# Kernel tuning notes

Hardware: AMD Instinct MI355X
Metric: run time of the kernel (lower is better)

## Reference

```python
import jax, jax.numpy as jnp
import numpy as np
from jax import lax

DILATIONS = (1, 3, 5)
EPS = 1e-5
B, T, C, S, K = 8, 4096, 512, 64, 3


def _adain(x, s, w, b):
    # instance norm over time (axis=1), per (batch, channel), no learned affine;
    # style-conditioned affine: (1+gamma)*xn + beta
    h = s @ w + b                              # (B, 2C)
    gamma, beta = jnp.split(h, 2, axis=-1)     # (B, C) each
    mu = jnp.mean(x, axis=1, keepdims=True)
    var = jnp.var(x, axis=1, keepdims=True)
    xn = (x - mu) * lax.rsqrt(var + EPS)
    return (1.0 + gamma[:, None, :]) * xn + beta[:, None, :]


def _snake(x, alpha):
    # snake activation: x + (1/a) * sin(a*x)^2
    return x + (1.0 / alpha) * jnp.sin(alpha * x) ** 2


def _wn_conv(x, v, g, b, dilation):
    # weight-normalized dilated 1d conv; v: (K, Cin, Cout), norm over (K, Cin)
    norm = jnp.sqrt(jnp.sum(v * v, axis=(0, 1), keepdims=True))
    w = g[None, None, :] * v / norm
    y = lax.conv_general_dilated(x, w, window_strides=(1,), padding='SAME',
                                 rhs_dilation=(dilation,),
                                 dimension_numbers=('NWC', 'WIO', 'NWC'))
    return y + b


def setup_inputs() -> dict:
    key = jax.random.key(0)
    ks = jax.random.split(key, 6)
    return {
        'x': jax.random.normal(ks[0], (B, T, C), dtype=jnp.float32),
        's': jax.random.normal(ks[1], (B, S), dtype=jnp.float32),
        'fc1_w': jax.random.normal(ks[2], (3, S, 2 * C), dtype=jnp.float32) * 0.02,
        'fc1_b': jnp.zeros((3, 2 * C), dtype=jnp.float32),
        'alpha1': jnp.ones((3, 1, 1, C), dtype=jnp.float32),
        'conv1_v': jax.random.normal(ks[3], (3, K, C, C), dtype=jnp.float32),
        'conv1_g': jnp.ones((3, C), dtype=jnp.float32),
        'conv1_b': jnp.zeros((3, C), dtype=jnp.float32),
        'fc2_w': jax.random.normal(ks[4], (3, S, 2 * C), dtype=jnp.float32) * 0.02,
        'fc2_b': jnp.zeros((3, 2 * C), dtype=jnp.float32),
        'alpha2': jnp.ones((3, 1, 1, C), dtype=jnp.float32),
        'conv2_v': jax.random.normal(ks[5], (3, K, C, C), dtype=jnp.float32),
        'conv2_g': jnp.ones((3, C), dtype=jnp.float32),
        'conv2_b': jnp.zeros((3, C), dtype=jnp.float32),
    }


def reference(x, s, fc1_w, fc1_b, alpha1, conv1_v, conv1_g, conv1_b,
              fc2_w, fc2_b, alpha2, conv2_v, conv2_g, conv2_b):
    for i, d in enumerate(DILATIONS):
        xt = _adain(x, s, fc1_w[i], fc1_b[i])
        xt = _snake(xt, alpha1[i])
        xt = _wn_conv(xt, conv1_v[i], conv1_g[i], conv1_b[i], d)
        xt = _adain(xt, s, fc2_w[i], fc2_b[i])
        xt = _snake(xt, alpha2[i])
        xt = _wn_conv(xt, conv2_v[i], conv2_g[i], conv2_b[i], 1)
        x = xt + x
    return x
```

## Files before the change

### kernel.cpp

```cpp
#include <hip/hip_runtime.h>
#include <hip/hip_bf16.h>

#define B_ 8
#define T_ 4096
#define C_ 512
#define S_ 64
#define KT 3
#define EPSC 1e-5f

typedef __attribute__((ext_vector_type(8))) short bf16x8;
typedef __attribute__((ext_vector_type(4))) float f32x4;

__device__ inline unsigned short f2bf(float x) {
    __hip_bfloat16 h = __float2bfloat16(x);
    return *reinterpret_cast<unsigned short*>(&h);
}

__global__ void norm_partial(const float* __restrict__ v1, const float* __restrict__ v2,
                             float* __restrict__ normsq) {
    int j = blockIdx.y;
    int i = j >> 1;
    const float* v = ((j & 1) ? v2 : v1) + (size_t)i * KT * C_ * C_;
    int r0 = blockIdx.x * 16;
    int tid = threadIdx.x;
    float a0 = 0.f, a1 = 0.f;
    for (int r = 0; r < 16; ++r) {
        const float* row = v + (size_t)(r0 + r) * C_;
        float x = row[tid];
        float y = row[tid + 256];
        a0 += x * x; a1 += y * y;
    }
    atomicAdd(&normsq[j * C_ + tid], a0);
    atomicAdd(&normsq[j * C_ + tid + 256], a1);
}

__global__ void wt_kernel(const float* __restrict__ v1, const float* __restrict__ v2,
                          const float* __restrict__ g1, const float* __restrict__ g2,
                          const float* __restrict__ normsq, unsigned short* __restrict__ wT) {
    __shared__ float tile[64][65];
    int jk = blockIdx.y;
    int j = jk / 3, k = jk % 3;
    int i = j >> 1;
    const float* v = ((j & 1) ? v2 : v1) + ((size_t)i * KT + k) * C_ * C_;
    const float* g = ((j & 1) ? g2 : g1) + (size_t)i * C_;
    int tci = (blockIdx.x >> 3) * 64;
    int tco = (blockIdx.x & 7) * 64;
    int tid = threadIdx.x;
    int lr = tid >> 6, lc = tid & 63;
    for (int rr = 0; rr < 16; ++rr) {
        int ci = rr * 4 + lr;
        tile[ci][lc] = v[(size_t)(tci + ci) * C_ + tco + lc];
    }
    __syncthreads();
    for (int rr = 0; rr < 16; ++rr) {
        int co_l = rr * 4 + lr;
        int co = tco + co_l;
        float w = g[co] * rsqrtf(normsq[j * C_ + co]) * tile[lc][co_l];
        wT[((size_t)j * KT + k) * C_ * C_ + (size_t)co * C_ + tci + lc] = f2bf(w);
    }
}

__global__ void stats_partial(const float* __restrict__ u, float* __restrict__ ssum,
                              float* __restrict__ ssq) {
    int c = blockIdx.y * 256 + threadIdx.x;
    int b = blockIdx.z;
    int t0 = blockIdx.x * 64;
    const float* p = u + ((size_t)b * T_ + t0) * C_ + c;
    float s1 = 0.f, s2 = 0.f;
    for (int t = 0; t < 64; ++t) {
        float x = p[(size_t)t * C_];
        s1 += x; s2 += x * x;
    }
    atomicAdd(&ssum[b * C_ + c], s1);
    atomicAdd(&ssq[b * C_ + c], s2);
}

__global__ void adain_finalize(const float* __restrict__ ssum, const float* __restrict__ ssq,
                               const float* __restrict__ s, const float* __restrict__ fcw,
                               const float* __restrict__ fcb,
                               float* __restrict__ scale, float* __restrict__ shift) {
    int idx = blockIdx.x * 256 + threadIdx.x;
    int b = idx >> 9, c = idx & (C_ - 1);
    float mu = ssum[idx] * (1.f / T_);
    float var = ssq[idx] * (1.f / T_) - mu * mu;
    var = fmaxf(var, 0.f);
    float gamma = fcb[c], beta = fcb[C_ + c];
    const float* sp = s + b * S_;
    for (int p = 0; p < S_; ++p) {
        float sv = sp[p];
        gamma += sv * fcw[p * 2 * C_ + c];
        beta  += sv * fcw[p * 2 * C_ + C_ + c];
    }
    float sc = (1.f + gamma) * rsqrtf(var + EPSC);
    scale[idx] = sc;
    shift[idx] = beta - mu * sc;
}

__global__ void act_kernel(const float* __restrict__ u, const float* __restrict__ scale,
                           const float* __restrict__ shift, const float* __restrict__ alpha,
                           unsigned short* __restrict__ z) {
    size_t idx4 = (size_t)blockIdx.x * 256 + threadIdx.x;
    size_t e0 = idx4 * 4;
    int c = (int)(e0 & (C_ - 1));
    int b = (int)(e0 >> 21);
    const float4 xv = *(const float4*)(u + e0);
    const float4 scv = *(const float4*)(scale + b * C_ + c);
    const float4 shv = *(const float4*)(shift + b * C_ + c);
    const float4 av = *(const float4*)(alpha + c);
    float xx[4] = {xv.x, xv.y, xv.z, xv.w};
    float ss[4] = {scv.x, scv.y, scv.z, scv.w};
    float hh[4] = {shv.x, shv.y, shv.z, shv.w};
    float aa[4] = {av.x, av.y, av.z, av.w};
    ushort4 o;
    unsigned short r[4];
    #pragma unroll
    for (int q = 0; q < 4; ++q) {
        float val = xx[q] * ss[q] + hh[q];
        float sn = sinf(aa[q] * val);
        r[q] = f2bf(val + sn * sn / aa[q]);
    }
    o.x = r[0]; o.y = r[1]; o.z = r[2]; o.w = r[3];
    *(ushort4*)(z + e0) = o;
}

#define BM 128
#define BN 128
#define HALO 5
#define AROWS (BM + 2 * HALO)
#define LSTR 40

__global__ __launch_bounds__(256) void conv_kernel(
    const unsigned short* __restrict__ z, const unsigned short* __restrict__ wT,
    const float* __restrict__ bias, const float* __restrict__ residual,
    float* __restrict__ out, int dil) {
    __shared__ unsigned short As[AROWS * LSTR];
    __shared__ unsigned short Bs[3 * BN * LSTR];
    int tid = threadIdx.x;
    int m0 = blockIdx.x * BM;
    int b = m0 >> 12;
    int t0 = m0 & (T_ - 1);
    int n0 = blockIdx.y * BN;
    int wv = tid >> 6;
    int l = tid & 63;
    int wm = (wv >> 1) * 64, wn = (wv & 1) * 64;
    int l16 = l & 15, lg = l >> 4;
    int ar = tid >> 2;
    int acol = (tid & 3) * 8;

    f32x4 acc[4][4];
    #pragma unroll
    for (int a = 0; a < 4; ++a)
        #pragma unroll
        for (int q = 0; q < 4; ++q) acc[a][q] = (f32x4){0.f, 0.f, 0.f, 0.f};

    for (int cc = 0; cc < C_; cc += 32) {
        #pragma unroll
        for (int it = 0; it < 3; ++it) {
            int r = ar + it * 64;
            if (r < AROWS) {
                int t = t0 - HALO + r;
                uint4 val = make_uint4(0u, 0u, 0u, 0u);
                if (t >= 0 && t < T_)
                    val = *(const uint4*)(z + ((size_t)b * T_ + t) * C_ + cc + acol);
                *(uint4*)(&As[r * LSTR + acol]) = val;
            }
        }
        #pragma unroll
        for (int it = 0; it < 6; ++it) {
            int r = ar + it * 64;
            int k = r >> 7, co = (r & 127) + n0;
            uint4 val = *(const uint4*)(wT + ((size_t)k * C_ + co) * C_ + cc + acol);
            *(uint4*)(&Bs[r * LSTR + acol]) = val;
        }
        __syncthreads();

        #pragma unroll
        for (int k = 0; k < 3; ++k) {
            int sh = (k - 1) * dil + HALO;
            bf16x8 afr[4], bfr[4];
            #pragma unroll
            for (int mf = 0; mf < 4; ++mf) {
                int row = wm + mf * 16 + l16 + sh;
                afr[mf] = *(const bf16x8*)(&As[row * LSTR + lg * 8]);
            }
            #pragma unroll
            for (int nf = 0; nf < 4; ++nf) {
                int co_l = wn + nf * 16 + l16;
                bfr[nf] = *(const bf16x8*)(&Bs[(k * BN + co_l) * LSTR + lg * 8]);
            }
            #pragma unroll
            for (int mf = 0; mf < 4; ++mf)
                #pragma unroll
                for (int nf = 0; nf < 4; ++nf)
                    acc[mf][nf] = __builtin_amdgcn_mfma_f32_16x16x32_bf16(
                        afr[mf], bfr[nf], acc[mf][nf], 0, 0, 0);
        }
        __syncthreads();
    }

    #pragma unroll
    for (int mf = 0; mf < 4; ++mf) {
        #pragma unroll
        for (int nf = 0; nf < 4; ++nf) {
            int co = n0 + wn + nf * 16 + l16;
            float bv = bias[co];
            #pragma unroll
            for (int r = 0; r < 4; ++r) {
                int t = t0 + wm + mf * 16 + lg * 4 + r;
                size_t idx = ((size_t)b * T_ + t) * C_ + co;
                float vres = residual ? residual[idx] : 0.f;
                out[idx] = acc[mf][nf][r] + bv + vres;
            }
        }
    }
}

extern "C" void kernel_launch(void* const* d_in, const int* in_sizes, int n_in,
                              void* d_out, int out_size, void* d_ws, size_t ws_size,
                              hipStream_t stream) {
    const float* x       = (const float*)d_in[0];
    const float* s       = (const float*)d_in[1];
    const float* fc1_w   = (const float*)d_in[2];
    const float* fc1_b   = (const float*)d_in[3];
    const float* alpha1  = (const float*)d_in[4];
    const float* conv1_v = (const float*)d_in[5];
    const float* conv1_g = (const float*)d_in[6];
    const float* conv1_b = (const float*)d_in[7];
    const float* fc2_w   = (const float*)d_in[8];
    const float* fc2_b   = (const float*)d_in[9];
    const float* alpha2  = (const float*)d_in[10];
    const float* conv2_v = (const float*)d_in[11];
    const float* conv2_g = (const float*)d_in[12];
    const float* conv2_b = (const float*)d_in[13];
    float* outp = (float*)d_out;

    char* ws = (char*)d_ws;
    const size_t MC = (size_t)B_ * T_ * C_;
    unsigned short* z  = (unsigned short*)ws;
    float* y1          = (float*)(ws + MC * 2);
    unsigned short* wT = (unsigned short*)(ws + MC * 2 + MC * 4);
    float* accum       = (float*)(ws + MC * 2 + MC * 4 + (size_t)6 * KT * C_ * C_ * 2);
    float* normsq = accum;
    float* stats  = accum + 6 * C_;
    float* scale  = stats + 12 * B_ * C_;
    float* shift  = scale + B_ * C_;

    hipMemsetAsync(accum, 0, (size_t)(6 * C_ + 12 * B_ * C_) * sizeof(float), stream);

    norm_partial<<<dim3(96, 6), 256, 0, stream>>>(conv1_v, conv2_v, normsq);
    wt_kernel<<<dim3(64, 18), 256, 0, stream>>>(conv1_v, conv2_v, conv1_g, conv2_g, normsq, wT);

    const int dils[3] = {1, 3, 5};
    const float* xin = x;
    for (int i = 0; i < 3; ++i) {
        float* s1 = stats + (size_t)(i * 2) * 2 * B_ * C_;
        float* s2 = s1 + B_ * C_;
        stats_partial<<<dim3(64, 2, 8), 256, 0, stream>>>(xin, s1, s2);
        adain_finalize<<<16, 256, 0, stream>>>(s1, s2, s, fc1_w + (size_t)i * S_ * 2 * C_,
                                               fc1_b + (size_t)i * 2 * C_, scale, shift);
        act_kernel<<<16384, 256, 0, stream>>>(xin, scale, shift, alpha1 + (size_t)i * C_, z);
        conv_kernel<<<dim3(256, 4), 256, 0, stream>>>(
            z, wT + (size_t)(i * 2) * KT * C_ * C_, conv1_b + (size_t)i * C_,
            nullptr, y1, dils[i]);

        s1 = stats + (size_t)(i * 2 + 1) * 2 * B_ * C_;
        s2 = s1 + B_ * C_;
        stats_partial<<<dim3(64, 2, 8), 256, 0, stream>>>(y1, s1, s2);
        adain_finalize<<<16, 256, 0, stream>>>(s1, s2, s, fc2_w + (size_t)i * S_ * 2 * C_,
                                               fc2_b + (size_t)i * 2 * C_, scale, shift);
        act_kernel<<<16384, 256, 0, stream>>>(y1, scale, shift, alpha2 + (size_t)i * C_, z);
        conv_kernel<<<dim3(256, 4), 256, 0, stream>>>(
            z, wT + (size_t)(i * 2 + 1) * KT * C_ * C_, conv2_b + (size_t)i * C_,
            xin, outp, 1);
        xin = outp;
    }
}
```

Before: 906.0 us.

## Pad activations, use direct-to-LDS loads with swizzle, fuse stats into conv epilogue

The activation buffer gets zero padding rows for each batch, which removes the bounds checks in the conv A-tile load. The conv kernel now uses global_load_lds with an XOR-swizzled 64-wide K tile, halving the number of K iterations and barriers. The conv epilogue also computes per-channel sum and sum-of-squares and atomically accumulates them, so all but the first stats_partial launch are removed along with their re-read of the output. The costs are extra atomics, a larger shared-memory footprint that can lower occupancy, and added complexity in the swizzle and padding layout.

```diff
diff --git a/kernel.cpp b/kernel.cpp
--- a/kernel.cpp
+++ b/kernel.cpp
@@ -7,9 +7,13 @@
 #define S_ 64
 #define KT 3
 #define EPSC 1e-5f
+#define PADB 5
+#define RB 4128
 
 typedef __attribute__((ext_vector_type(8))) short bf16x8;
 typedef __attribute__((ext_vector_type(4))) float f32x4;
+typedef __attribute__((address_space(3))) unsigned int lds_u32_t;
+typedef const __attribute__((address_space(1))) unsigned int glb_u32_t;
 
 __device__ inline unsigned short f2bf(float x) {
     __hip_bfloat16 h = __float2bfloat16(x);
@@ -60,6 +64,16 @@
     }
 }
 
+__global__ void zero_pads(unsigned short* __restrict__ zp) {
+    int q = blockIdx.x * 256 + threadIdx.x;
+    int b = q >> 11, r = q & 2047;
+    int row = r >> 6;
+    int col = (r & 63) * 8;
+    int prow = row < PADB ? row : row + T_;
+    uint4 zz = make_uint4(0u, 0u, 0u, 0u);
+    *(uint4*)(zp + ((size_t)b * RB + prow) * C_ + col) = zz;
+}
+
 __global__ void stats_partial(const float* __restrict__ u, float* __restrict__ ssum,
                               float* __restrict__ ssq) {
     int c = blockIdx.y * 256 + threadIdx.x;
@@ -98,7 +112,7 @@
 
 __global__ void act_kernel(const float* __restrict__ u, const float* __restrict__ scale,
                            const float* __restrict__ shift, const float* __restrict__ alpha,
-                           unsigned short* __restrict__ z) {
+                           unsigned short* __restrict__ zp) {
     size_t idx4 = (size_t)blockIdx.x * 256 + threadIdx.x;
     size_t e0 = idx4 * 4;
     int c = (int)(e0 & (C_ - 1));
@@ -120,21 +134,20 @@
         r[q] = f2bf(val + sn * sn / aa[q]);
     }
     o.x = r[0]; o.y = r[1]; o.z = r[2]; o.w = r[3];
-    *(ushort4*)(z + e0) = o;
+    size_t dst = ((size_t)b * RB + PADB) * C_ + (e0 & (((size_t)1 << 21) - 1));
+    *(ushort4*)(zp + dst) = o;
 }
 
 #define BM 128
 #define BN 128
-#define HALO 5
-#define AROWS (BM + 2 * HALO)
-#define LSTR 40
+#define AR 160
 
 __global__ __launch_bounds__(256) void conv_kernel(
-    const unsigned short* __restrict__ z, const unsigned short* __restrict__ wT,
+    const unsigned short* __restrict__ zp, const unsigned short* __restrict__ wT,
     const float* __restrict__ bias, const float* __restrict__ residual,
-    float* __restrict__ out, int dil) {
-    __shared__ unsigned short As[AROWS * LSTR];
-    __shared__ unsigned short Bs[3 * BN * LSTR];
+    float* __restrict__ out, float* __restrict__ ssum, float* __restrict__ ssq, int dil) {
+    __shared__ unsigned short As[AR * 64];
+    __shared__ unsigned short Bs[3 * BN * 64];
     int tid = threadIdx.x;
     int m0 = blockIdx.x * BM;
     int b = m0 >> 12;
@@ -144,8 +157,9 @@
     int l = tid & 63;
     int wm = (wv >> 1) * 64, wn = (wv & 1) * 64;
     int l16 = l & 15, lg = l >> 4;
-    int ar = tid >> 2;
-    int acol = (tid & 3) * 8;
+
+    const unsigned short* aBase = zp + ((size_t)b * RB + t0) * C_;
+    const unsigned short* bBase = wT + (size_t)n0 * C_;
 
     f32x4 acc[4][4];
     #pragma unroll
@@ -153,64 +167,75 @@
         #pragma unroll
         for (int q = 0; q < 4; ++q) acc[a][q] = (f32x4){0.f, 0.f, 0.f, 0.f};
 
-    for (int cc = 0; cc < C_; cc += 32) {
-        #pragma unroll
-        for (int it = 0; it < 3; ++it) {
-            int r = ar + it * 64;
-            if (r < AROWS) {
-                int t = t0 - HALO + r;
-                uint4 val = make_uint4(0u, 0u, 0u, 0u);
-                if (t >= 0 && t < T_)
-                    val = *(const uint4*)(z + ((size_t)b * T_ + t) * C_ + cc + acol);
-                *(uint4*)(&As[r * LSTR + acol]) = val;
+    for (int ci0 = 0; ci0 < C_; ci0 += 64) {
+        #pragma unroll
+        for (int it = 0; it < 5; ++it) {
+            int chunk = it * 256 + tid;
+            int row = chunk >> 3, c = chunk & 7;
+            const unsigned short* src = aBase + (size_t)row * C_ + ci0 + ((c ^ (row & 7)) * 8);
+            __builtin_amdgcn_global_load_lds((glb_u32_t*)src,
+                (lds_u32_t*)&As[(it * 256 + wv * 64) * 8], 16, 0, 0);
+        }
+        #pragma unroll
+        for (int it = 0; it < 12; ++it) {
+            int chunk = it * 256 + tid;
+            int row = chunk >> 3, c = chunk & 7;
+            int k = row >> 7, co = row & 127;
+            const unsigned short* src = bBase + ((size_t)k * C_ + co) * C_ + ci0 + ((c ^ (row & 7)) * 8);
+            __builtin_amdgcn_global_load_lds((glb_u32_t*)src,
+                (lds_u32_t*)&Bs[(it * 256 + wv * 64) * 8], 16, 0, 0);
+        }
+        __syncthreads();
+
+        #pragma unroll
+        for (int ks = 0; ks < 2; ++ks) {
+            #pragma unroll
+            for (int k = 0; k < 3; ++k) {
+                int sh = (k - 1) * dil + PADB;
+                bf16x8 afr[4], bfr[4];
+                #pragma unroll
+                for (int mf = 0; mf < 4; ++mf) {
+                    int row = wm + mf * 16 + l16 + sh;
+                    afr[mf] = *(const bf16x8*)(&As[row * 64 + (((ks * 4 + lg) ^ (row & 7)) * 8)]);
+                }
+                #pragma unroll
+                for (int nf = 0; nf < 4; ++nf) {
+                    int row = wn + nf * 16 + l16;
+                    bfr[nf] = *(const bf16x8*)(&Bs[(k * BN + row) * 64 + (((ks * 4 + lg) ^ (row & 7)) * 8)]);
+                }
+                #pragma unroll
+                for (int mf = 0; mf < 4; ++mf)
+                    #pragma unroll
+                    for (int nf = 0; nf < 4; ++nf)
+                        acc[mf][nf] = __builtin_amdgcn_mfma_f32_16x16x32_bf16(
+                            afr[mf], bfr[nf], acc[mf][nf], 0, 0, 0);
             }
         }
-        #pragma unroll
-        for (int it = 0; it < 6; ++it) {
-            int r = ar + it * 64;
-            int k = r >> 7, co = (r & 127) + n0;
-            uint4 val = *(const uint4*)(wT + ((size_t)k * C_ + co) * C_ + cc + acol);
-            *(uint4*)(&Bs[r * LSTR + acol]) = val;
-        }
         __syncthreads();
-
-        #pragma unroll
-        for (int k = 0; k < 3; ++k) {
-            int sh = (k - 1) * dil + HALO;
-            bf16x8 afr[4], bfr[4];
-            #pragma unroll
-            for (int mf = 0; mf < 4; ++mf) {
-                int row = wm + mf * 16 + l16 + sh;
-                afr[mf] = *(const bf16x8*)(&As[row * LSTR + lg * 8]);
-            }
-            #pragma unroll
-            for (int nf = 0; nf < 4; ++nf) {
-                int co_l = wn + nf * 16 + l16;
-                bfr[nf] = *(const bf16x8*)(&Bs[(k * BN + co_l) * LSTR + lg * 8]);
-            }
-            #pragma unroll
-            for (int mf = 0; mf < 4; ++mf)
-                #pragma unroll
-                for (int nf = 0; nf < 4; ++nf)
-                    acc[mf][nf] = __builtin_amdgcn_mfma_f32_16x16x32_bf16(
-                        afr[mf], bfr[nf], acc[mf][nf], 0, 0, 0);
-        }
-        __syncthreads();
     }
 
     #pragma unroll
-    for (int mf = 0; mf < 4; ++mf) {
-        #pragma unroll
-        for (int nf = 0; nf < 4; ++nf) {
-            int co = n0 + wn + nf * 16 + l16;
-            float bv = bias[co];
+    for (int nf = 0; nf < 4; ++nf) {
+        int co = n0 + wn + nf * 16 + l16;
+        float bv = bias[co];
+        float s1 = 0.f, s2 = 0.f;
+        #pragma unroll
+        for (int mf = 0; mf < 4; ++mf) {
             #pragma unroll
             for (int r = 0; r < 4; ++r) {
                 int t = t0 + wm + mf * 16 + lg * 4 + r;
                 size_t idx = ((size_t)b * T_ + t) * C_ + co;
-                float vres = residual ? residual[idx] : 0.f;
-                out[idx] = acc[mf][nf][r] + bv + vres;
+                float val = acc[mf][nf][r] + bv;
+                if (residual) val += residual[idx];
+                out[idx] = val;
+                s1 += val; s2 += val * val;
             }
+        }
+        s1 += __shfl_xor(s1, 16); s1 += __shfl_xor(s1, 32);
+        s2 += __shfl_xor(s2, 16); s2 += __shfl_xor(s2, 32);
+        if (lg == 0) {
+            atomicAdd(&ssum[b * C_ + co], s1);
+            atomicAdd(&ssq[b * C_ + co], s2);
         }
     }
 }
@@ -236,42 +261,46 @@
 
     char* ws = (char*)d_ws;
     const size_t MC = (size_t)B_ * T_ * C_;
+    const size_t ZSZ = (size_t)B_ * RB * C_ * 2;
     unsigned short* z  = (unsigned short*)ws;
-    float* y1          = (float*)(ws + MC * 2);
-    unsigned short* wT = (unsigned short*)(ws + MC * 2 + MC * 4);
-    float* accum       = (float*)(ws + MC * 2 + MC * 4 + (size_t)6 * KT * C_ * C_ * 2);
+    float* y1          = (float*)(ws + ZSZ);
+    unsigned short* wT = (unsigned short*)(ws + ZSZ + MC * 4);
+    float* accum       = (float*)(ws + ZSZ + MC * 4 + (size_t)6 * KT * C_ * C_ * 2);
     float* normsq = accum;
     float* stats  = accum + 6 * C_;
-    float* scale  = stats + 12 * B_ * C_;
+    float* scale  = stats + 7 * 2 * B_ * C_;
     float* shift  = scale + B_ * C_;
 
-    hipMemsetAsync(accum, 0, (size_t)(6 * C_ + 12 * B_ * C_) * sizeof(float), stream);
-
+    hipMemsetAsync(accum, 0, (size_t)(6 * C_ + 7 * 2 * B_ * C_) * sizeof(float), stream);
+    zero_pads<<<64, 256, 0, stream>>>(z);
     norm_partial<<<dim3(96, 6), 256, 0, stream>>>(conv1_v, conv2_v, normsq);
     wt_kernel<<<dim3(64, 18), 256, 0, stream>>>(conv1_v, conv2_v, conv1_g, conv2_g, normsq, wT);
 
     const int dils[3] = {1, 3, 5};
     const float* xin = x;
+    const int BC = B_ * C_;
+    stats_partial<<<dim3(64, 2, 8), 256, 0, stream>>>(x, stats, stats + BC);
+
     for (int i = 0; i < 3; ++i) {
-        float* s1 = stats + (size_t)(i * 2) * 2 * B_ * C_;
-        float* s2 = s1 + B_ * C_;
-        stats_partial<<<dim3(64, 2, 8), 256, 0, stream>>>(xin, s1, s2);
-        adain_finalize<<<16, 256, 0, stream>>>(s1, s2, s, fc1_w + (size_t)i * S_ * 2 * C_,
+        float* p_in  = stats + (size_t)(2 * i) * 2 * BC;
+        float* p_mid = stats + (size_t)(2 * i + 1) * 2 * BC;
+        float* p_out = stats + (size_t)(2 * i + 2) * 2 * BC;
+
+        adain_finalize<<<16, 256, 0, stream>>>(p_in, p_in + BC, s,
+                                               fc1_w + (size_t)i * S_ * 2 * C_,
                                                fc1_b + (size_t)i * 2 * C_, scale, shift);
         act_kernel<<<16384, 256, 0, stream>>>(xin, scale, shift, alpha1 + (size_t)i * C_, z);
         conv_kernel<<<dim3(256, 4), 256, 0, stream>>>(
             z, wT + (size_t)(i * 2) * KT * C_ * C_, conv1_b + (size_t)i * C_,
-            nullptr, y1, dils[i]);
-
-        s1 = stats + (size_t)(i * 2 + 1) * 2 * B_ * C_;
-        s2 = s1 + B_ * C_;
-        stats_partial<<<dim3(64, 2, 8), 256, 0, stream>>>(y1, s1, s2);
-        adain_finalize<<<16, 256, 0, stream>>>(s1, s2, s, fc2_w + (size_t)i * S_ * 2 * C_,
+            nullptr, y1, p_mid, p_mid + BC, dils[i]);
+
+        adain_finalize<<<16, 256, 0, stream>>>(p_mid, p_mid + BC, s,
+                                               fc2_w + (size_t)i * S_ * 2 * C_,
                                                fc2_b + (size_t)i * 2 * C_, scale, shift);
         act_kernel<<<16384, 256, 0, stream>>>(y1, scale, shift, alpha2 + (size_t)i * C_, z);
         conv_kernel<<<dim3(256, 4), 256, 0, stream>>>(
             z, wT + (size_t)(i * 2 + 1) * KT * C_ * C_, conv2_b + (size_t)i * C_,
-            xin, outp, 1);
+            xin, outp, p_out, p_out + BC, 1);
         xin = outp;
     }
 }
```

Result: faster. 769.5 us (-15.1%).
